# Kernel optimization log

Measured on AMD Instinct MI355X. Metric: run time of the kernel, lower is better.

## Reference

```python
import jax, jax.numpy as jnp
import numpy as np

B, S, D, H = 2, 2048, 1024, 16
HD = D // H  # head_dim = 64


def setup_inputs() -> dict:
    key = jax.random.key(0)
    ks = jax.random.split(key, 12)
    sc = 1.0 / np.sqrt(D)
    return {
        "query": jax.random.normal(ks[0], (B, S, D), jnp.float32),
        "key_": jax.random.normal(ks[1], (B, S, D), jnp.float32),
        "value": jax.random.normal(ks[2], (B, S, D), jnp.float32),
        "mask": jax.random.randint(ks[3], (B, 1, S, S), 0, 2, jnp.int32),
        "Wq": jax.random.normal(ks[4], (D, D), jnp.float32) * sc,
        "bq": jnp.zeros((D,), jnp.float32),
        "Wk": jax.random.normal(ks[5], (D, D), jnp.float32) * sc,
        "bk": jnp.zeros((D,), jnp.float32),
        "Wv": jax.random.normal(ks[6], (D, D), jnp.float32) * sc,
        "bv": jnp.zeros((D,), jnp.float32),
        "Wo": jax.random.normal(ks[7], (D, D), jnp.float32) * sc,
        "bo": jnp.zeros((D,), jnp.float32),
    }


def _split(x):
    # [B, S, D] -> [B, H, S, HD]
    return x.reshape(B, S, H, HD).transpose(0, 2, 1, 3)


def reference(query, key_, value, mask, Wq, bq, Wk, bk, Wv, bv, Wo, bo):
    Q = _split(query @ Wq + bq)
    K = _split(key_ @ Wk + bk)
    V = _split(value @ Wv + bv)
    # scores: [B, H, Sq, Sk]
    scores = jnp.einsum("bhqd,bhkd->bhqk", Q, K) / jnp.sqrt(jnp.float32(HD))
    scores = jnp.where(mask == 0, jnp.float32(-1e9), scores)
    probs = jax.nn.softmax(scores, axis=-1)
    attn = jnp.einsum("bhqk,bhkd->bhqd", probs, V)
    out = attn.transpose(0, 2, 1, 3).reshape(B, S, D)
    return out @ Wo + bo
```

## Files before the change

kernel.cpp:

```cpp
#include <hip/hip_runtime.h>
#include <stdint.h>

typedef _Float16 f16;
typedef _Float16 f16x4 __attribute__((ext_vector_type(4)));
typedef _Float16 f16x8 __attribute__((ext_vector_type(8)));
typedef __fp16 hf16x2 __attribute__((ext_vector_type(2)));
typedef float f32x4 __attribute__((ext_vector_type(4)));
typedef float f32x16 __attribute__((ext_vector_type(16)));
typedef unsigned u32;
typedef unsigned uint2v __attribute__((ext_vector_type(2)));

static constexpr int Bb = 2, Ss = 2048, Dd = 1024, Hh = 16, HDd = 64;
static constexpr int M_ROWS = Bb * Ss;

static constexpr size_t OFF_WT  = 24ull << 20;
static constexpr size_t OFF_QKV = 32ull << 20;
static constexpr size_t OFF_ATT = 56ull << 20;
static constexpr size_t OFF_MB  = 64ull << 20;

__device__ __forceinline__ void gll16(const void* g, void* l) {
  __builtin_amdgcn_global_load_lds((__attribute__((address_space(1))) const void*)g,
                                   (__attribute__((address_space(3))) void*)l, 16, 0, 0);
}

__device__ __forceinline__ int lds_byte(int row, int slot) {
  return row * 128 + (((slot ^ (row & 7)) & 7) << 4);
}

__device__ __forceinline__ float ex2(float x) {
  float r; asm("v_exp_f32 %0, %1" : "=v"(r) : "v"(x)); return r;
}

union H2U { hf16x2 h; u32 u; };

__global__ __launch_bounds__(256) void prep(const int* __restrict__ mask,
                                            unsigned* __restrict__ bits,
                                            const float* __restrict__ wq,
                                            const float* __restrict__ wk,
                                            const float* __restrict__ wv,
                                            const float* __restrict__ wo,
                                            f16* __restrict__ wt) {
  const int bid = blockIdx.x;
  __shared__ float t[32][33];
  if (bid < 32768) {
    size_t i = (size_t)bid * 256 + threadIdx.x;
    int v = mask[i];
    unsigned long long bm = __ballot(v != 0);
    if ((threadIdx.x & 63) == 0) {
      size_t w = i >> 5;
      bits[w]     = (unsigned)bm;
      bits[w + 1] = (unsigned)(bm >> 32);
    }
  } else {
    const int wb = bid - 32768;
    const int z = wb >> 10, by = (wb >> 5) & 31, bx = wb & 31;
    const float* W = z == 0 ? wq : z == 1 ? wk : z == 2 ? wv : wo;
    f16* Wt = wt + (size_t)z * Dd * Dd;
    const int tx = threadIdx.x & 31, ty = threadIdx.x >> 5;
    const int k0 = by * 32, n0 = bx * 32;
    for (int i = 0; i < 32; i += 8) t[ty + i][tx] = W[(size_t)(k0 + ty + i) * Dd + n0 + tx];
    __syncthreads();
    for (int i = 0; i < 32; i += 8) Wt[(size_t)(n0 + ty + i) * Dd + k0 + tx] = (f16)t[tx][ty + i];
  }
}

__global__ __launch_bounds__(256) void gemm_qkv(const float* __restrict__ qin,
                                                const float* __restrict__ kin,
                                                const float* __restrict__ vin,
                                                const f16* __restrict__ Btbase,
                                                const float* __restrict__ b0,
                                                const float* __restrict__ b1,
                                                const float* __restrict__ b2,
                                                f16* __restrict__ Cbase) {
  constexpr int K = Dd, N = Dd;
  const int f = blockIdx.x;
  const int z = f >> 8, i = f & 255;
  const int xg = i & 7, sl = i >> 3;
  const int m0 = (xg * 4 + (sl >> 3)) * 128, n0 = (sl & 7) * 128;
  const float* A = z == 0 ? qin : z == 1 ? kin : vin;
  const f16* Bt = Btbase + (size_t)z * N * K;
  const float* bias = z == 0 ? b0 : z == 1 ? b1 : b2;
  __shared__ f16 As[128 * 64], Bs[128 * 64];
  const int tid = threadIdx.x, l = tid & 63, w = tid >> 6;
  const int li = l & 15, gq = l >> 4;
  const int wm = (w >> 1) * 64, wn = (w & 1) * 64;
  const int sr = l >> 3, ss = l & 7;
  const int scol = ((ss ^ sr) << 3);

  f32x4 acc[4][4];
  for (int mi = 0; mi < 4; mi++)
    for (int ni = 0; ni < 4; ni++) acc[mi][ni] = f32x4{0.f, 0.f, 0.f, 0.f};

  float4 a0[4], a1[4];
#pragma unroll
  for (int c = 0; c < 4; c++) {
    int r = (w * 4 + c) * 8 + sr;
    const float* src = A + (size_t)(m0 + r) * K + scol;
    a0[c] = *(const float4*)src; a1[c] = *(const float4*)(src + 4);
  }

  for (int kt = 0; kt < K; kt += 64) {
    if (kt) __syncthreads();
#pragma unroll
    for (int c = 0; c < 4; c++) {
      const int chunk = w * 4 + c;
      H2U h0, h1, h2, h3;
      h0.h = __builtin_amdgcn_cvt_pkrtz(a0[c].x, a0[c].y);
      h1.h = __builtin_amdgcn_cvt_pkrtz(a0[c].z, a0[c].w);
      h2.h = __builtin_amdgcn_cvt_pkrtz(a1[c].x, a1[c].y);
      h3.h = __builtin_amdgcn_cvt_pkrtz(a1[c].z, a1[c].w);
      union { u32 uu[4]; f16x8 v8; } pk;
      pk.uu[0] = h0.u; pk.uu[1] = h1.u; pk.uu[2] = h2.u; pk.uu[3] = h3.u;
      *(f16x8*)((char*)As + chunk * 1024 + l * 16) = pk.v8;
      int r = chunk * 8 + sr;
      gll16(Bt + (size_t)(n0 + r) * K + kt + scol, (char*)Bs + chunk * 1024);
    }
    __syncthreads();
    if (kt + 64 < K) {
#pragma unroll
      for (int c = 0; c < 4; c++) {
        int r = (w * 4 + c) * 8 + sr;
        const float* src = A + (size_t)(m0 + r) * K + (kt + 64) + scol;
        a0[c] = *(const float4*)src; a1[c] = *(const float4*)(src + 4);
      }
    }
#pragma unroll
    for (int ks = 0; ks < 2; ks++) {
      f16x8 af[4], bf[4];
#pragma unroll
      for (int ii = 0; ii < 4; ii++) {
        af[ii] = *(const f16x8*)((const char*)As + lds_byte(wm + ii * 16 + li, ks * 4 + gq));
        bf[ii] = *(const f16x8*)((const char*)Bs + lds_byte(wn + ii * 16 + li, ks * 4 + gq));
      }
#pragma unroll
      for (int mi = 0; mi < 4; mi++)
#pragma unroll
        for (int ni = 0; ni < 4; ni++)
          acc[mi][ni] = __builtin_amdgcn_mfma_f32_16x16x32_f16(af[mi], bf[ni], acc[mi][ni], 0, 0, 0);
    }
  }

  const float scl = (z == 0) ? 0.18033688011112042f : 1.0f;
  if (z == 2) {
    f16* Vt = Cbase + (size_t)2 * M_ROWS * N;
#pragma unroll
    for (int mi = 0; mi < 4; mi++)
#pragma unroll
      for (int ni = 0; ni < 4; ni++) {
        const int col = n0 + wn + ni * 16 + li;
        const int r0  = m0 + wm + mi * 16 + gq * 4;
        const int bb_ = r0 >> 11, s = r0 & 2047;
        const float bv = bias[col];
        f16x4 pk;
#pragma unroll
        for (int j = 0; j < 4; j++) pk[j] = (f16)(acc[mi][ni][j] + bv);
        *(f16x4*)(Vt + ((size_t)(bb_ * Hh) << 17) + (size_t)col * Ss + s) = pk;
      }
  } else {
    for (int mi = 0; mi < 4; mi++)
      for (int ni = 0; ni < 4; ni++) {
        const int r0  = m0 + wm + mi * 16 + gq * 4;
        const int col = n0 + wn + ni * 16 + li;
        const float bb = bias[col];
#pragma unroll
        for (int j = 0; j < 4; j++) {
          float val = (acc[mi][ni][j] + bb) * scl;
          Cbase[(size_t)z * M_ROWS * N + (size_t)(r0 + j) * N + col] = (f16)val;
        }
      }
  }
}

__global__ __launch_bounds__(256) void gemm_out(const f16* __restrict__ A,
                                                const f16* __restrict__ Bt,
                                                const float* __restrict__ bias,
                                                float* __restrict__ C) {
  constexpr int K = Dd, N = Dd;
  const int f = blockIdx.x;
  const int xg = f & 7, sl = f >> 3;
  const int m0 = (xg * 4 + (sl >> 3)) * 128, n0 = (sl & 7) * 128;
  __shared__ f16 As[128 * 64], Bs[128 * 64];
  const int tid = threadIdx.x, l = tid & 63, w = tid >> 6;
  const int li = l & 15, gq = l >> 4;
  const int wm = (w >> 1) * 64, wn = (w & 1) * 64;
  const int sr = l >> 3, ss = l & 7;
  const int scol = ((ss ^ sr) << 3);

  f32x4 acc[4][4];
  for (int mi = 0; mi < 4; mi++)
    for (int ni = 0; ni < 4; ni++) acc[mi][ni] = f32x4{0.f, 0.f, 0.f, 0.f};

  for (int kt = 0; kt < K; kt += 64) {
    __syncthreads();
    for (int c = 0; c < 4; c++) {
      int chunk = w * 4 + c;
      int r = chunk * 8 + sr;
      gll16(A  + (size_t)(m0 + r) * K + kt + scol, (char*)As + chunk * 1024);
      gll16(Bt + (size_t)(n0 + r) * K + kt + scol, (char*)Bs + chunk * 1024);
    }
    __syncthreads();
#pragma unroll
    for (int ks = 0; ks < 2; ks++) {
      f16x8 af[4], bf[4];
#pragma unroll
      for (int ii = 0; ii < 4; ii++) {
        af[ii] = *(const f16x8*)((const char*)As + lds_byte(wm + ii * 16 + li, ks * 4 + gq));
        bf[ii] = *(const f16x8*)((const char*)Bs + lds_byte(wn + ii * 16 + li, ks * 4 + gq));
      }
#pragma unroll
      for (int mi = 0; mi < 4; mi++)
#pragma unroll
        for (int ni = 0; ni < 4; ni++)
          acc[mi][ni] = __builtin_amdgcn_mfma_f32_16x16x32_f16(af[mi], bf[ni], acc[mi][ni], 0, 0, 0);
    }
  }
  for (int mi = 0; mi < 4; mi++)
    for (int ni = 0; ni < 4; ni++) {
      const int r0  = m0 + wm + mi * 16 + gq * 4;
      const int col = n0 + wn + ni * 16 + li;
      const float bb = bias[col];
#pragma unroll
      for (int j = 0; j < 4; j++)
        C[(size_t)(r0 + j) * N + col] = acc[mi][ni][j] + bb;
    }
}

__global__ __launch_bounds__(512, 4) void attn_fused(const f16* __restrict__ Qp,
                                                     const f16* __restrict__ Kp,
                                                     const f16* __restrict__ Vt,
                                                     const u32* __restrict__ mbits,
                                                     f16* __restrict__ outp) {
  const int flat = blockIdx.x;
  const int xcd = flat & 7, jj = flat >> 3;
  const int qt = jj & 15;
  const int hb = xcd * 4 + (jj >> 4);
  const int h = hb & 15, b = hb >> 4;

  const int tid = threadIdx.x, l = tid & 63, w = tid >> 6;
  const int lo = l & 31, hi = l >> 5;
  const int half = w >> 2, wsub = w & 3;
  const int q0 = qt * 128, wq = wsub * 32;

  __shared__ char smem[65536];
  char* hbase = smem + half * 32768;
  char* Qst = smem + 16384;

  const size_t qkbase = (size_t)b * Ss * Dd + (size_t)h * HDd;
  const f16* Vtb = Vt + (size_t)(b * Hh + h) * HDd * Ss;
  const int sr = l >> 3, ss = l & 7;
  const int scol = ((ss ^ sr) << 3);

  for (int c = 0; c < 2; c++) {
    int chunk = w * 2 + c, r = chunk * 8 + sr;
    gll16(Qp + qkbase + (size_t)(q0 + r) * Dd + scol, Qst + chunk * 1024);
  }
  const int kt0 = half * 16;
  for (int c = 0; c < 2; c++) {
    int chunk = wsub * 2 + c, r = chunk * 8 + sr;
    gll16(Kp + qkbase + (size_t)(kt0 * 64 + r) * Dd + scol, hbase + chunk * 1024);
    gll16(Vtb + (size_t)r * Ss + kt0 * 64 + scol, hbase + 8192 + chunk * 1024);
  }
  __syncthreads();

  f16x8 qf[4];
#pragma unroll
  for (int c = 0; c < 4; c++)
    qf[c] = *(const f16x8*)(Qst + lds_byte(wq + lo, 2 * c + hi));
  __syncthreads();

  f32x16 accO0 = {0}, accO1 = {0};
  float m_run = -1e30f, l_run = 0.f;
  const u32* mrow = mbits + (size_t)(b * Ss + q0 + wq + lo) * 64;

  for (int it = 0; it < 16; it++) {
    const int kt = kt0 + it;
    if (it) __syncthreads();
    char* bufc = hbase + (it & 1) * 16384;
    if (it < 15) {
      char* bufn = hbase + ((it + 1) & 1) * 16384;
      const int k0n = (kt + 1) * 64;
      for (int c = 0; c < 2; c++) {
        int chunk = wsub * 2 + c, r = chunk * 8 + sr;
        gll16(Kp + qkbase + (size_t)(k0n + r) * Dd + scol, bufn + chunk * 1024);
        gll16(Vtb + (size_t)r * Ss + k0n + scol, bufn + 8192 + chunk * 1024);
      }
    }
    const char* Kb = bufc;
    const char* Vb = bufc + 8192;

    f32x16 s0 = {0}, s1 = {0};
    __builtin_amdgcn_s_setprio(1);
#pragma unroll
    for (int c = 0; c < 4; c++) {
      f16x8 kf0 = *(const f16x8*)(Kb + lds_byte(lo, 2 * c + hi));
      f16x8 kf1 = *(const f16x8*)(Kb + lds_byte(32 + lo, 2 * c + hi));
      s0 = __builtin_amdgcn_mfma_f32_32x32x16_f16(kf0, qf[c], s0, 0, 0, 0);
      s1 = __builtin_amdgcn_mfma_f32_32x32x16_f16(kf1, qf[c], s1, 0, 0, 0);
    }
    __builtin_amdgcn_s_setprio(0);

    uint2v mw = *(const uint2v*)(mrow + kt * 2);
    u32 wa = mw.x >> (hi << 2);
    u32 wb = mw.y >> (hi << 2);

    float x0 = fmaxf(s0[0], s1[0]), x1 = fmaxf(s0[1], s1[1]);
    float x2 = fmaxf(s0[2], s1[2]), x3 = fmaxf(s0[3], s1[3]);
#pragma unroll
    for (int r = 4; r < 16; r += 4) {
      x0 = fmaxf(x0, fmaxf(s0[r],     s1[r]));
      x1 = fmaxf(x1, fmaxf(s0[r + 1], s1[r + 1]));
      x2 = fmaxf(x2, fmaxf(s0[r + 2], s1[r + 2]));
      x3 = fmaxf(x3, fmaxf(s0[r + 3], s1[r + 3]));
    }
    float pm = fmaxf(fmaxf(x0, x1), fmaxf(x2, x3));

    float mn;
    if (__all(pm <= m_run + 11.5f)) {
      mn = m_run;
    } else {
      pm = fmaxf(pm, __shfl_xor(pm, 32));
      mn = fmaxf(m_run, pm);
      const float so = ex2(m_run - mn);
      m_run = mn;
      l_run *= so;
      accO0 *= so; accO1 *= so;
    }

    float racc = 0.f;
#pragma unroll
    for (int r = 0; r < 16; r++) {
      const int kk = (r & 3) + 8 * (r >> 2);
      u32 ma = (u32)(((int)(wa << (31 - kk))) >> 31);
      u32 mb = (u32)(((int)(wb << (31 - kk))) >> 31);
      float e0 = __uint_as_float(__float_as_uint(ex2(s0[r] - mn)) & ma);
      float e1 = __uint_as_float(__float_as_uint(ex2(s1[r] - mn)) & mb);
      s0[r] = e0; s1[r] = e1;
      racc += e0 + e1;
    }
    l_run += racc;

    u32 pw[16];
#pragma unroll
    for (int j = 0; j < 8; j++) {
      H2U a, c;
      a.h = __builtin_amdgcn_cvt_pkrtz(s0[2 * j], s0[2 * j + 1]);
      c.h = __builtin_amdgcn_cvt_pkrtz(s1[2 * j], s1[2 * j + 1]);
      pw[j] = a.u; pw[8 + j] = c.u;
    }
#pragma unroll
    for (int c = 0; c < 4; c++) {
      asm volatile("v_permlane32_swap_b32 %0, %1" : "+v"(pw[4 * c]), "+v"(pw[4 * c + 2]));
      asm volatile("v_permlane32_swap_b32 %0, %1" : "+v"(pw[4 * c + 1]), "+v"(pw[4 * c + 3]));
    }

    __builtin_amdgcn_s_setprio(1);
#pragma unroll
    for (int c = 0; c < 4; c++) {
      union { u32 u[4]; f16x8 v; } pu;
      pu.u[0] = pw[4 * c]; pu.u[1] = pw[4 * c + 1];
      pu.u[2] = pw[4 * c + 2]; pu.u[3] = pw[4 * c + 3];
      f16x8 vf0 = *(const f16x8*)(Vb + lds_byte(lo, 2 * c + hi));
      f16x8 vf1 = *(const f16x8*)(Vb + lds_byte(32 + lo, 2 * c + hi));
      accO0 = __builtin_amdgcn_mfma_f32_32x32x16_f16(vf0, pu.v, accO0, 0, 0, 0);
      accO1 = __builtin_amdgcn_mfma_f32_32x32x16_f16(vf1, pu.v, accO1, 0, 0, 0);
    }
    __builtin_amdgcn_s_setprio(0);
  }

  __syncthreads();
  float* mg = (float*)smem;
  if (half == 1) {
    float* p = mg + (size_t)(wsub * 64 + l) * 35;
#pragma unroll
    for (int r = 0; r < 16; r++) { p[r] = accO0[r]; p[16 + r] = accO1[r]; }
    p[32] = m_run; p[33] = l_run;
  }
  __syncthreads();
  if (half == 1) return;

  const float* p = mg + (size_t)(wsub * 64 + l) * 35;
  const float mB = p[32], lB = p[33];
  const float m = fmaxf(m_run, mB);
  const float fA = ex2(m_run - m), fB = ex2(mB - m);
  float lmerged = l_run * fA + lB * fB;
#pragma unroll
  for (int r = 0; r < 16; r++) {
    accO0[r] = accO0[r] * fA + p[r] * fB;
    accO1[r] = accO1[r] * fA + p[16 + r] * fB;
  }
  const float lf = lmerged + __shfl_xor(lmerged, 32);
  const float inv = 1.0f / lf;

  char* Ot = smem + 40960 + wsub * 4096;
#pragma unroll
  for (int j = 0; j < 8; j++) {
    H2U pk;
    pk.h = __builtin_amdgcn_cvt_pkrtz(accO0[2 * j] * inv, accO0[2 * j + 1] * inv);
    int slot = (j >> 1);
    int addr = lo * 128 + (((slot ^ (lo & 7)) & 7) << 4) + 4 * (j & 1) + 8 * hi;
    *(u32*)(Ot + addr) = pk.u;
  }
#pragma unroll
  for (int j = 0; j < 8; j++) {
    H2U pk;
    pk.h = __builtin_amdgcn_cvt_pkrtz(accO1[2 * j] * inv, accO1[2 * j + 1] * inv);
    int slot = (j >> 1) + 4;
    int addr = lo * 128 + (((slot ^ (lo & 7)) & 7) << 4) + 4 * (j & 1) + 8 * hi;
    *(u32*)(Ot + addr) = pk.u;
  }
  asm volatile("s_waitcnt lgkmcnt(0)" ::: "memory");
  {
    const int q = l >> 1, halfq = l & 1;
    f16* gbase = outp + qkbase + (size_t)(q0 + wq + q) * Dd + halfq * 32;
#pragma unroll
    for (int c = 0; c < 4; c++) {
      int byte = q * 128 + ((((halfq * 4 + c) ^ (q & 7)) & 7) << 4);
      f16x8 v = *(const f16x8*)(Ot + byte);
      *(f16x8*)(gbase + c * 8) = v;
    }
  }
}

extern "C" void kernel_launch(void* const* d_in, const int* in_sizes, int n_in,
                              void* d_out, int out_size, void* d_ws, size_t ws_size,
                              hipStream_t stream) {
  const float* query = (const float*)d_in[0];
  const float* key_  = (const float*)d_in[1];
  const float* value = (const float*)d_in[2];
  const int*   mask  = (const int*)d_in[3];
  const float* Wq = (const float*)d_in[4];
  const float* bq = (const float*)d_in[5];
  const float* Wk = (const float*)d_in[6];
  const float* bk = (const float*)d_in[7];
  const float* Wv = (const float*)d_in[8];
  const float* bv = (const float*)d_in[9];
  const float* Wo = (const float*)d_in[10];
  const float* bo = (const float*)d_in[11];

  char* ws = (char*)d_ws;
  f16* Wt  = (f16*)(ws + OFF_WT);
  f16* QKV = (f16*)(ws + OFF_QKV);
  f16* ATT = (f16*)(ws + OFF_ATT);
  unsigned* MB = (unsigned*)(ws + OFF_MB);

  prep<<<dim3(32768 + 4096), 256, 0, stream>>>(mask, MB, Wq, Wk, Wv, Wo, Wt);
  gemm_qkv<<<dim3(768), 256, 0, stream>>>(query, key_, value, Wt, bq, bk, bv, QKV);
  attn_fused<<<dim3(512), 512, 0, stream>>>(QKV, QKV + (size_t)M_ROWS * Dd,
                                            QKV + 2 * (size_t)M_ROWS * Dd, MB, ATT);
  gemm_out<<<dim3(256), 256, 0, stream>>>(ATT, Wt + 3 * (size_t)Dd * Dd, bo, (float*)d_out);
}
```

Baseline: 146.0 us.

## Split K across two wave groups in QKV and output GEMMs with LDS reduction

```diff
diff --git a/kernel.cpp b/kernel.cpp
--- a/kernel.cpp
+++ b/kernel.cpp
@@ -64,14 +64,14 @@
   }
 }
 
-__global__ __launch_bounds__(256) void gemm_qkv(const float* __restrict__ qin,
-                                                const float* __restrict__ kin,
-                                                const float* __restrict__ vin,
-                                                const f16* __restrict__ Btbase,
-                                                const float* __restrict__ b0,
-                                                const float* __restrict__ b1,
-                                                const float* __restrict__ b2,
-                                                f16* __restrict__ Cbase) {
+__global__ __launch_bounds__(512, 4) void gemm_qkv(const float* __restrict__ qin,
+                                                   const float* __restrict__ kin,
+                                                   const float* __restrict__ vin,
+                                                   const f16* __restrict__ Btbase,
+                                                   const float* __restrict__ b0,
+                                                   const float* __restrict__ b1,
+                                                   const float* __restrict__ b2,
+                                                   f16* __restrict__ Cbase) {
   constexpr int K = Dd, N = Dd;
   const int f = blockIdx.x;
   const int z = f >> 8, i = f & 255;
@@ -80,10 +80,14 @@
   const float* A = z == 0 ? qin : z == 1 ? kin : vin;
   const f16* Bt = Btbase + (size_t)z * N * K;
   const float* bias = z == 0 ? b0 : z == 1 ? b1 : b2;
-  __shared__ f16 As[128 * 64], Bs[128 * 64];
+
+  __shared__ char smem[65536];
   const int tid = threadIdx.x, l = tid & 63, w = tid >> 6;
+  const int half = w >> 2, wsub = w & 3;
+  char* As = smem + half * 32768;
+  char* Bs = As + 16384;
   const int li = l & 15, gq = l >> 4;
-  const int wm = (w >> 1) * 64, wn = (w & 1) * 64;
+  const int wm = (wsub >> 1) * 64, wn = (wsub & 1) * 64;
   const int sr = l >> 3, ss = l & 7;
   const int scol = ((ss ^ sr) << 3);
 
@@ -91,46 +95,39 @@
   for (int mi = 0; mi < 4; mi++)
     for (int ni = 0; ni < 4; ni++) acc[mi][ni] = f32x4{0.f, 0.f, 0.f, 0.f};
 
-  float4 a0[4], a1[4];
-#pragma unroll
-  for (int c = 0; c < 4; c++) {
-    int r = (w * 4 + c) * 8 + sr;
-    const float* src = A + (size_t)(m0 + r) * K + scol;
-    a0[c] = *(const float4*)src; a1[c] = *(const float4*)(src + 4);
-  }
-
-  for (int kt = 0; kt < K; kt += 64) {
-    if (kt) __syncthreads();
-#pragma unroll
-    for (int c = 0; c < 4; c++) {
-      const int chunk = w * 4 + c;
+  const int kb = half * 512;
+  for (int it = 0; it < 8; it++) {
+    const int kt = kb + it * 64;
+    if (it) __syncthreads();
+#pragma unroll
+    for (int c = 0; c < 4; c++) {
+      int chunk = wsub * 4 + c;
+      int r = chunk * 8 + sr;
+      gll16(Bt + (size_t)(n0 + r) * K + kt + scol, Bs + chunk * 1024);
+    }
+#pragma unroll
+    for (int c = 0; c < 4; c++) {
+      int chunk = wsub * 4 + c;
+      int r = chunk * 8 + sr;
+      const float* src = A + (size_t)(m0 + r) * K + kt + scol;
+      float4 v0 = *(const float4*)src, v1 = *(const float4*)(src + 4);
       H2U h0, h1, h2, h3;
-      h0.h = __builtin_amdgcn_cvt_pkrtz(a0[c].x, a0[c].y);
-      h1.h = __builtin_amdgcn_cvt_pkrtz(a0[c].z, a0[c].w);
-      h2.h = __builtin_amdgcn_cvt_pkrtz(a1[c].x, a1[c].y);
-      h3.h = __builtin_amdgcn_cvt_pkrtz(a1[c].z, a1[c].w);
+      h0.h = __builtin_amdgcn_cvt_pkrtz(v0.x, v0.y);
+      h1.h = __builtin_amdgcn_cvt_pkrtz(v0.z, v0.w);
+      h2.h = __builtin_amdgcn_cvt_pkrtz(v1.x, v1.y);
+      h3.h = __builtin_amdgcn_cvt_pkrtz(v1.z, v1.w);
       union { u32 uu[4]; f16x8 v8; } pk;
       pk.uu[0] = h0.u; pk.uu[1] = h1.u; pk.uu[2] = h2.u; pk.uu[3] = h3.u;
-      *(f16x8*)((char*)As + chunk * 1024 + l * 16) = pk.v8;
-      int r = chunk * 8 + sr;
-      gll16(Bt + (size_t)(n0 + r) * K + kt + scol, (char*)Bs + chunk * 1024);
+      *(f16x8*)(As + chunk * 1024 + l * 16) = pk.v8;
     }
     __syncthreads();
-    if (kt + 64 < K) {
-#pragma unroll
-      for (int c = 0; c < 4; c++) {
-        int r = (w * 4 + c) * 8 + sr;
-        const float* src = A + (size_t)(m0 + r) * K + (kt + 64) + scol;
-        a0[c] = *(const float4*)src; a1[c] = *(const float4*)(src + 4);
-      }
-    }
 #pragma unroll
     for (int ks = 0; ks < 2; ks++) {
       f16x8 af[4], bf[4];
 #pragma unroll
       for (int ii = 0; ii < 4; ii++) {
-        af[ii] = *(const f16x8*)((const char*)As + lds_byte(wm + ii * 16 + li, ks * 4 + gq));
-        bf[ii] = *(const f16x8*)((const char*)Bs + lds_byte(wn + ii * 16 + li, ks * 4 + gq));
+        af[ii] = *(const f16x8*)(As + lds_byte(wm + ii * 16 + li, ks * 4 + gq));
+        bf[ii] = *(const f16x8*)(Bs + lds_byte(wn + ii * 16 + li, ks * 4 + gq));
       }
 #pragma unroll
       for (int mi = 0; mi < 4; mi++)
@@ -139,6 +136,22 @@
           acc[mi][ni] = __builtin_amdgcn_mfma_f32_16x16x32_f16(af[mi], bf[ni], acc[mi][ni], 0, 0, 0);
     }
   }
+
+  __syncthreads();
+  if (half == 1) {
+#pragma unroll
+    for (int mi = 0; mi < 4; mi++)
+#pragma unroll
+      for (int ni = 0; ni < 4; ni++)
+        *(f32x4*)(smem + wsub * 16384 + (mi * 4 + ni) * 1024 + l * 16) = acc[mi][ni];
+  }
+  __syncthreads();
+  if (half == 1) return;
+#pragma unroll
+  for (int mi = 0; mi < 4; mi++)
+#pragma unroll
+    for (int ni = 0; ni < 4; ni++)
+      acc[mi][ni] += *(const f32x4*)(smem + wsub * 16384 + (mi * 4 + ni) * 1024 + l * 16);
 
   const float scl = (z == 0) ? 0.18033688011112042f : 1.0f;
   if (z == 2) {
@@ -171,18 +184,21 @@
   }
 }
 
-__global__ __launch_bounds__(256) void gemm_out(const f16* __restrict__ A,
-                                                const f16* __restrict__ Bt,
-                                                const float* __restrict__ bias,
-                                                float* __restrict__ C) {
+__global__ __launch_bounds__(512, 4) void gemm_out(const f16* __restrict__ A,
+                                                   const f16* __restrict__ Bt,
+                                                   const float* __restrict__ bias,
+                                                   float* __restrict__ C) {
   constexpr int K = Dd, N = Dd;
   const int f = blockIdx.x;
   const int xg = f & 7, sl = f >> 3;
   const int m0 = (xg * 4 + (sl >> 3)) * 128, n0 = (sl & 7) * 128;
-  __shared__ f16 As[128 * 64], Bs[128 * 64];
+  __shared__ char smem[65536];
   const int tid = threadIdx.x, l = tid & 63, w = tid >> 6;
+  const int half = w >> 2, wsub = w & 3;
+  char* As = smem + half * 32768;
+  char* Bs = As + 16384;
   const int li = l & 15, gq = l >> 4;
-  const int wm = (w >> 1) * 64, wn = (w & 1) * 64;
+  const int wm = (wsub >> 1) * 64, wn = (wsub & 1) * 64;
   const int sr = l >> 3, ss = l & 7;
   const int scol = ((ss ^ sr) << 3);
 
@@ -190,13 +206,16 @@
   for (int mi = 0; mi < 4; mi++)
     for (int ni = 0; ni < 4; ni++) acc[mi][ni] = f32x4{0.f, 0.f, 0.f, 0.f};
 
-  for (int kt = 0; kt < K; kt += 64) {
-    __syncthreads();
-    for (int c = 0; c < 4; c++) {
-      int chunk = w * 4 + c;
+  const int kb = half * 512;
+  for (int it = 0; it < 8; it++) {
+    const int kt = kb + it * 64;
+    if (it) __syncthreads();
+#pragma unroll
+    for (int c = 0; c < 4; c++) {
+      int chunk = wsub * 4 + c;
       int r = chunk * 8 + sr;
-      gll16(A  + (size_t)(m0 + r) * K + kt + scol, (char*)As + chunk * 1024);
-      gll16(Bt + (size_t)(n0 + r) * K + kt + scol, (char*)Bs + chunk * 1024);
+      gll16(A  + (size_t)(m0 + r) * K + kt + scol, As + chunk * 1024);
+      gll16(Bt + (size_t)(n0 + r) * K + kt + scol, Bs + chunk * 1024);
     }
     __syncthreads();
 #pragma unroll
@@ -204,8 +223,8 @@
       f16x8 af[4], bf[4];
 #pragma unroll
       for (int ii = 0; ii < 4; ii++) {
-        af[ii] = *(const f16x8*)((const char*)As + lds_byte(wm + ii * 16 + li, ks * 4 + gq));
-        bf[ii] = *(const f16x8*)((const char*)Bs + lds_byte(wn + ii * 16 + li, ks * 4 + gq));
+        af[ii] = *(const f16x8*)(As + lds_byte(wm + ii * 16 + li, ks * 4 + gq));
+        bf[ii] = *(const f16x8*)(Bs + lds_byte(wn + ii * 16 + li, ks * 4 + gq));
       }
 #pragma unroll
       for (int mi = 0; mi < 4; mi++)
@@ -214,6 +233,23 @@
           acc[mi][ni] = __builtin_amdgcn_mfma_f32_16x16x32_f16(af[mi], bf[ni], acc[mi][ni], 0, 0, 0);
     }
   }
+
+  __syncthreads();
+  if (half == 1) {
+#pragma unroll
+    for (int mi = 0; mi < 4; mi++)
+#pragma unroll
+      for (int ni = 0; ni < 4; ni++)
+        *(f32x4*)(smem + wsub * 16384 + (mi * 4 + ni) * 1024 + l * 16) = acc[mi][ni];
+  }
+  __syncthreads();
+  if (half == 1) return;
+#pragma unroll
+  for (int mi = 0; mi < 4; mi++)
+#pragma unroll
+    for (int ni = 0; ni < 4; ni++)
+      acc[mi][ni] += *(const f32x4*)(smem + wsub * 16384 + (mi * 4 + ni) * 1024 + l * 16);
+
   for (int mi = 0; mi < 4; mi++)
     for (int ni = 0; ni < 4; ni++) {
       const int r0  = m0 + wm + mi * 16 + gq * 4;
@@ -444,8 +480,8 @@
   unsigned* MB = (unsigned*)(ws + OFF_MB);
 
   prep<<<dim3(32768 + 4096), 256, 0, stream>>>(mask, MB, Wq, Wk, Wv, Wo, Wt);
-  gemm_qkv<<<dim3(768), 256, 0, stream>>>(query, key_, value, Wt, bq, bk, bv, QKV);
+  gemm_qkv<<<dim3(768), 512, 0, stream>>>(query, key_, value, Wt, bq, bk, bv, QKV);
   attn_fused<<<dim3(512), 512, 0, stream>>>(QKV, QKV + (size_t)M_ROWS * Dd,
                                             QKV + 2 * (size_t)M_ROWS * Dd, MB, ATT);
-  gemm_out<<<dim3(256), 256, 0, stream>>>(ATT, Wt + 3 * (size_t)Dd * Dd, bo, (float*)d_out);
-}
+  gemm_out<<<dim3(256), 512, 0, stream>>>(ATT, Wt + 3 * (size_t)Dd * Dd, bo, (float*)d_out);
+}
```

After: 148.3 us. About the same (+1.6%).

## Double-buffer LDS tiles in QKV and output projection GEMMs

Applied to the files above, without the earlier changes.

```diff
diff --git a/kernel.cpp b/kernel.cpp
--- a/kernel.cpp
+++ b/kernel.cpp
@@ -80,7 +80,8 @@
   const float* A = z == 0 ? qin : z == 1 ? kin : vin;
   const f16* Bt = Btbase + (size_t)z * N * K;
   const float* bias = z == 0 ? b0 : z == 1 ? b1 : b2;
-  __shared__ f16 As[128 * 64], Bs[128 * 64];
+
+  __shared__ char smem[65536];
   const int tid = threadIdx.x, l = tid & 63, w = tid >> 6;
   const int li = l & 15, gq = l >> 4;
   const int wm = (w >> 1) * 64, wn = (w & 1) * 64;
@@ -94,33 +95,38 @@
   float4 a0[4], a1[4];
 #pragma unroll
   for (int c = 0; c < 4; c++) {
-    int r = (w * 4 + c) * 8 + sr;
+    int chunk = w * 4 + c, r = chunk * 8 + sr;
+    gll16(Bt + (size_t)(n0 + r) * K + scol, smem + 16384 + chunk * 1024);
     const float* src = A + (size_t)(m0 + r) * K + scol;
     a0[c] = *(const float4*)src; a1[c] = *(const float4*)(src + 4);
   }
-
-  for (int kt = 0; kt < K; kt += 64) {
-    if (kt) __syncthreads();
-#pragma unroll
-    for (int c = 0; c < 4; c++) {
-      const int chunk = w * 4 + c;
-      H2U h0, h1, h2, h3;
-      h0.h = __builtin_amdgcn_cvt_pkrtz(a0[c].x, a0[c].y);
-      h1.h = __builtin_amdgcn_cvt_pkrtz(a0[c].z, a0[c].w);
-      h2.h = __builtin_amdgcn_cvt_pkrtz(a1[c].x, a1[c].y);
-      h3.h = __builtin_amdgcn_cvt_pkrtz(a1[c].z, a1[c].w);
-      union { u32 uu[4]; f16x8 v8; } pk;
-      pk.uu[0] = h0.u; pk.uu[1] = h1.u; pk.uu[2] = h2.u; pk.uu[3] = h3.u;
-      *(f16x8*)((char*)As + chunk * 1024 + l * 16) = pk.v8;
-      int r = chunk * 8 + sr;
-      gll16(Bt + (size_t)(n0 + r) * K + kt + scol, (char*)Bs + chunk * 1024);
-    }
+#pragma unroll
+  for (int c = 0; c < 4; c++) {
+    int chunk = w * 4 + c;
+    H2U h0, h1, h2, h3;
+    h0.h = __builtin_amdgcn_cvt_pkrtz(a0[c].x, a0[c].y);
+    h1.h = __builtin_amdgcn_cvt_pkrtz(a0[c].z, a0[c].w);
+    h2.h = __builtin_amdgcn_cvt_pkrtz(a1[c].x, a1[c].y);
+    h3.h = __builtin_amdgcn_cvt_pkrtz(a1[c].z, a1[c].w);
+    union { u32 uu[4]; f16x8 v8; } pk;
+    pk.uu[0] = h0.u; pk.uu[1] = h1.u; pk.uu[2] = h2.u; pk.uu[3] = h3.u;
+    *(f16x8*)(smem + chunk * 1024 + l * 16) = pk.v8;
+  }
+
+  int cur = 0;
+  for (int it = 0; it < 16; it++) {
     __syncthreads();
-    if (kt + 64 < K) {
+    char* Asc = smem + cur * 32768;
+    char* Bsc = Asc + 16384;
+    char* Asn = smem + (cur ^ 1) * 32768;
+    char* Bsn = Asn + 16384;
+    if (it < 15) {
+      const int kn = (it + 1) * 64;
 #pragma unroll
       for (int c = 0; c < 4; c++) {
-        int r = (w * 4 + c) * 8 + sr;
-        const float* src = A + (size_t)(m0 + r) * K + (kt + 64) + scol;
+        int chunk = w * 4 + c, r = chunk * 8 + sr;
+        gll16(Bt + (size_t)(n0 + r) * K + kn + scol, Bsn + chunk * 1024);
+        const float* src = A + (size_t)(m0 + r) * K + kn + scol;
         a0[c] = *(const float4*)src; a1[c] = *(const float4*)(src + 4);
       }
     }
@@ -129,8 +135,8 @@
       f16x8 af[4], bf[4];
 #pragma unroll
       for (int ii = 0; ii < 4; ii++) {
-        af[ii] = *(const f16x8*)((const char*)As + lds_byte(wm + ii * 16 + li, ks * 4 + gq));
-        bf[ii] = *(const f16x8*)((const char*)Bs + lds_byte(wn + ii * 16 + li, ks * 4 + gq));
+        af[ii] = *(const f16x8*)(Asc + lds_byte(wm + ii * 16 + li, ks * 4 + gq));
+        bf[ii] = *(const f16x8*)(Bsc + lds_byte(wn + ii * 16 + li, ks * 4 + gq));
       }
 #pragma unroll
       for (int mi = 0; mi < 4; mi++)
@@ -138,6 +144,21 @@
         for (int ni = 0; ni < 4; ni++)
           acc[mi][ni] = __builtin_amdgcn_mfma_f32_16x16x32_f16(af[mi], bf[ni], acc[mi][ni], 0, 0, 0);
     }
+    if (it < 15) {
+#pragma unroll
+      for (int c = 0; c < 4; c++) {
+        int chunk = w * 4 + c;
+        H2U h0, h1, h2, h3;
+        h0.h = __builtin_amdgcn_cvt_pkrtz(a0[c].x, a0[c].y);
+        h1.h = __builtin_amdgcn_cvt_pkrtz(a0[c].z, a0[c].w);
+        h2.h = __builtin_amdgcn_cvt_pkrtz(a1[c].x, a1[c].y);
+        h3.h = __builtin_amdgcn_cvt_pkrtz(a1[c].z, a1[c].w);
+        union { u32 uu[4]; f16x8 v8; } pk;
+        pk.uu[0] = h0.u; pk.uu[1] = h1.u; pk.uu[2] = h2.u; pk.uu[3] = h3.u;
+        *(f16x8*)(Asn + chunk * 1024 + l * 16) = pk.v8;
+      }
+    }
+    cur ^= 1;
   }
 
   const float scl = (z == 0) ? 0.18033688011112042f : 1.0f;
@@ -179,7 +200,7 @@
   const int f = blockIdx.x;
   const int xg = f & 7, sl = f >> 3;
   const int m0 = (xg * 4 + (sl >> 3)) * 128, n0 = (sl & 7) * 128;
-  __shared__ f16 As[128 * 64], Bs[128 * 64];
+  __shared__ char smem[65536];
   const int tid = threadIdx.x, l = tid & 63, w = tid >> 6;
   const int li = l & 15, gq = l >> 4;
   const int wm = (w >> 1) * 64, wn = (w & 1) * 64;
@@ -190,22 +211,35 @@
   for (int mi = 0; mi < 4; mi++)
     for (int ni = 0; ni < 4; ni++) acc[mi][ni] = f32x4{0.f, 0.f, 0.f, 0.f};
 
-  for (int kt = 0; kt < K; kt += 64) {
+#pragma unroll
+  for (int c = 0; c < 4; c++) {
+    int chunk = w * 4 + c, r = chunk * 8 + sr;
+    gll16(A  + (size_t)(m0 + r) * K + scol, smem + chunk * 1024);
+    gll16(Bt + (size_t)(n0 + r) * K + scol, smem + 16384 + chunk * 1024);
+  }
+
+  int cur = 0;
+  for (int it = 0; it < 16; it++) {
     __syncthreads();
-    for (int c = 0; c < 4; c++) {
-      int chunk = w * 4 + c;
-      int r = chunk * 8 + sr;
-      gll16(A  + (size_t)(m0 + r) * K + kt + scol, (char*)As + chunk * 1024);
-      gll16(Bt + (size_t)(n0 + r) * K + kt + scol, (char*)Bs + chunk * 1024);
-    }
-    __syncthreads();
+    char* Asc = smem + cur * 32768;
+    char* Bsc = Asc + 16384;
+    if (it < 15) {
+      char* Asn = smem + (cur ^ 1) * 32768;
+      const int kn = (it + 1) * 64;
+#pragma unroll
+      for (int c = 0; c < 4; c++) {
+        int chunk = w * 4 + c, r = chunk * 8 + sr;
+        gll16(A  + (size_t)(m0 + r) * K + kn + scol, Asn + chunk * 1024);
+        gll16(Bt + (size_t)(n0 + r) * K + kn + scol, Asn + 16384 + chunk * 1024);
+      }
+    }
 #pragma unroll
     for (int ks = 0; ks < 2; ks++) {
       f16x8 af[4], bf[4];
 #pragma unroll
       for (int ii = 0; ii < 4; ii++) {
-        af[ii] = *(const f16x8*)((const char*)As + lds_byte(wm + ii * 16 + li, ks * 4 + gq));
-        bf[ii] = *(const f16x8*)((const char*)Bs + lds_byte(wn + ii * 16 + li, ks * 4 + gq));
+        af[ii] = *(const f16x8*)(Asc + lds_byte(wm + ii * 16 + li, ks * 4 + gq));
+        bf[ii] = *(const f16x8*)(Bsc + lds_byte(wn + ii * 16 + li, ks * 4 + gq));
       }
 #pragma unroll
       for (int mi = 0; mi < 4; mi++)
@@ -213,7 +247,9 @@
         for (int ni = 0; ni < 4; ni++)
           acc[mi][ni] = __builtin_amdgcn_mfma_f32_16x16x32_f16(af[mi], bf[ni], acc[mi][ni], 0, 0, 0);
     }
-  }
+    cur ^= 1;
+  }
+
   for (int mi = 0; mi < 4; mi++)
     for (int ni = 0; ni < 4; ni++) {
       const int r0  = m0 + wm + mi * 16 + gq * 4;
```

After: 138.1 us. -5.4%, faster.
